# Kernel tuning notes

Measured on AMD Instinct MI355X. Metric: run time of the kernel, lower is better.

Reference implementation:

```python
import jax, jax.numpy as jnp
import numpy as np

INPUT_DIM = 64
INNER_DIM = 64
BATCH = 32768


def setup_inputs() -> dict:
    key = jax.random.key(0)
    ks = jax.random.split(key, 9)
    D, I = INPUT_DIM, INNER_DIM
    s1 = 1.0  # Linear(1, inner): fan_in=1
    s2 = 1.0 / np.sqrt(I)
    sg1 = 1.0 / np.sqrt(D * I)
    sg2 = 1.0 / np.sqrt(I)
    return {
        "x": jax.random.normal(ks[0], (BATCH, D), dtype=jnp.float32),
        # per-feature psi params, stacked over feature dim D
        "W1": jax.random.uniform(ks[1], (D, I), jnp.float32, -s1, s1),   # Linear(1, inner) weight
        "b1": jax.random.uniform(ks[2], (D, I), jnp.float32, -s1, s1),
        "W2": jax.random.uniform(ks[3], (D, I, I), jnp.float32, -s2, s2),  # Linear(inner, inner)
        "b2": jax.random.uniform(ks[4], (D, I), jnp.float32, -s2, s2),
        # g params
        "Wg1": jax.random.uniform(ks[5], (D * I, I), jnp.float32, -sg1, sg1),
        "bg1": jax.random.uniform(ks[6], (I,), jnp.float32, -sg1, sg1),
        "Wg2": jax.random.uniform(ks[7], (I, 1), jnp.float32, -sg2, sg2),
        "bg2": jax.random.uniform(ks[8], (1,), jnp.float32, -sg2, sg2),
    }


def reference(x, W1, b1, W2, b2, Wg1, bg1, Wg2, bg2):
    B = x.shape[0]
    # all psi_i first layers as one broadcasted outer product: [B, D, I]
    h = jnp.tanh(x[:, :, None] * W1[None, :, :] + b1[None, :, :])
    # per-feature second Linear(inner, inner): batched matmul over D
    psi = jnp.einsum("bdi,dio->bdo", h, W2) + b2[None, :, :]
    psi_concat = psi.reshape(B, -1)  # [B, D*I] == torch.cat over features
    hg = jnp.tanh(psi_concat @ Wg1 + bg1)
    out = hg @ Wg2 + bg2  # [B, 1]
    return out
```

## Files before the change

### kernel.cpp

```cpp
#include <hip/hip_runtime.h>
#include <stdint.h>

#define BATCH 32768
#define TANH_C 2.8853900817779268f

typedef __attribute__((ext_vector_type(8))) short short8;
typedef __attribute__((ext_vector_type(4))) float f32x4;
typedef __attribute__((ext_vector_type(4))) unsigned int u32x4;

__device__ __forceinline__ uint16_t bf16_rtne(float f) {
    union { float f; uint32_t u; } v; v.f = f;
    uint32_t u = v.u;
    u += 0x7fffu + ((u >> 16) & 1u);
    return (uint16_t)(u >> 16);
}

#if defined(__has_builtin)
#if __has_builtin(__builtin_amdgcn_cvt_pk_bf16_f32)
#define HAVE_CVT_PK_BF16 1
#endif
#endif

__device__ __forceinline__ uint32_t pack2_bf16(float a, float b) {
#ifdef HAVE_CVT_PK_BF16
    auto v = __builtin_amdgcn_cvt_pk_bf16_f32(a, b);
    uint32_t r; __builtin_memcpy(&r, &v, 4); return r;
#else
    return (uint32_t)bf16_rtne(a) | ((uint32_t)bf16_rtne(b) << 16);
#endif
}

__device__ __forceinline__ float tanh_pre(float a) {
    float e = __builtin_amdgcn_exp2f(a);
    return 1.0f - 2.0f * __builtin_amdgcn_rcpf(1.0f + e);
}

__device__ __forceinline__ float fast_tanh(float x) {
    return tanh_pre(x * TANH_C);
}

__global__ __launch_bounds__(512) void kol_pack(const float* __restrict__ W2,
                                                const float* __restrict__ Wg1,
                                                uint16_t* __restrict__ Bp) {
    __shared__ __align__(16) float w2t[64 * 65];
    __shared__ __align__(16) float g1s[64 * 64];

    const int t = threadIdx.x;
    const int d = blockIdx.x;

    for (int f = t * 4; f < 4096; f += 2048) {
        float4 v = *(const float4*)&W2[(size_t)d * 4096 + f];
        int j = f >> 6, o = f & 63;
        w2t[(o + 0) * 65 + j] = v.x;
        w2t[(o + 1) * 65 + j] = v.y;
        w2t[(o + 2) * 65 + j] = v.z;
        w2t[(o + 3) * 65 + j] = v.w;
        *(float4*)&g1s[f] = *(const float4*)&Wg1[(size_t)d * 4096 + f];
    }
    __syncthreads();

    const int jg = t >> 6;
    const int n  = t & 63;
    float acc[8];
#pragma unroll
    for (int i = 0; i < 8; ++i) acc[i] = 0.f;

#pragma unroll 4
    for (int o = 0; o < 64; ++o) {
        float g = g1s[o * 64 + n];
        const float* w = &w2t[o * 65 + jg * 8];
#pragma unroll
        for (int jj = 0; jj < 8; ++jj) acc[jj] = fmaf(w[jj], g, acc[jj]);
    }

    u32x4 pk;
    pk.x = pack2_bf16(acc[0], acc[1]);
    pk.y = pack2_bf16(acc[2], acc[3]);
    pk.z = pack2_bf16(acc[4], acc[5]);
    pk.w = pack2_bf16(acc[6], acc[7]);
    int off = ((d * 2 + (jg >> 2)) * 4 + (n >> 4)) * 64 + (jg & 3) * 16 + (n & 15);
    ((u32x4*)Bp)[off] = pk;
}

__global__ __launch_bounds__(1024) void kol_cg(const float* __restrict__ b2,
                                               const float* __restrict__ Wg1,
                                               const float* __restrict__ bg1,
                                               float* __restrict__ cg) {
    __shared__ float red[16][64];
    const int t = threadIdx.x;
    const int n = t & 63, seg = t >> 6;
    float a = 0.f;
    const int m0 = seg * 256;
#pragma unroll 4
    for (int m = m0; m < m0 + 256; ++m)
        a = fmaf(b2[m], Wg1[(size_t)m * 64 + n], a);
    red[seg][n] = a;
    __syncthreads();
    if (t < 64) {
        float s = bg1[n];
#pragma unroll
        for (int r = 0; r < 16; ++r) s += red[r][n];
        cg[n] = s;
    }
}

__global__ __launch_bounds__(512, 2) void kol_main(
    const float* __restrict__ x, const float* __restrict__ W1, const float* __restrict__ b1,
    const uint16_t* __restrict__ Bp, const float* __restrict__ cg,
    const float* __restrict__ Wg2, const float* __restrict__ bg2f,
    float* __restrict__ out) {
    __shared__ __align__(16) float xs[128 * 68];
    __shared__ __align__(16) float w1s[4096];
    __shared__ __align__(16) float b1s[4096];

    const int tid = threadIdx.x;
    const int wave = tid >> 6, lane = tid & 63;
    const int quad = lane >> 4, lm = lane & 15;
    const int rowbase = blockIdx.x * 128;

    for (int f = tid * 4; f < 8192; f += 2048) {
        int r = f >> 6, c = f & 63;
        float4 v = *(const float4*)&x[(size_t)(rowbase + r) * 64 + c];
        v.x *= TANH_C; v.y *= TANH_C; v.z *= TANH_C; v.w *= TANH_C;
        *(float4*)&xs[r * 68 + c] = v;
    }
    for (int f = tid * 4; f < 4096; f += 2048) {
        *(float4*)&w1s[f] = *(const float4*)&W1[f];
        float4 b = *(const float4*)&b1[f];
        b.x *= TANH_C; b.y *= TANH_C; b.z *= TANH_C; b.w *= TANH_C;
        *(float4*)&b1s[f] = b;
    }
    __syncthreads();

    f32x4 acc[4];
#pragma unroll
    for (int nt = 0; nt < 4; ++nt) acc[nt] = (f32x4){0.f, 0.f, 0.f, 0.f};

    const int myrow = wave * 16 + lm;
    const float* xrow = &xs[myrow * 68];
    const short8* bbase = (const short8*)Bp + lane;

    for (int d = 0; d < 64; ++d) {
        const short8* bp = bbase + (size_t)d * 8 * 64;
        short8 bf[8];
#pragma unroll
        for (int i = 0; i < 8; ++i) bf[i] = bp[i * 64];

        const float xv = xrow[d];
        const float* wq = &w1s[d * 64 + quad * 8];
        const float* bq = &b1s[d * 64 + quad * 8];
        float4 wA = *(const float4*)&wq[0];
        float4 wB = *(const float4*)&wq[4];
        float4 wC = *(const float4*)&wq[32];
        float4 wD = *(const float4*)&wq[36];
        float4 bA = *(const float4*)&bq[0];
        float4 bB = *(const float4*)&bq[4];
        float4 bC = *(const float4*)&bq[32];
        float4 bD = *(const float4*)&bq[36];

        union { short8 s; uint32_t u[4]; } a0, a1;
        a0.u[0] = pack2_bf16(tanh_pre(fmaf(xv, wA.x, bA.x)), tanh_pre(fmaf(xv, wA.y, bA.y)));
        a0.u[1] = pack2_bf16(tanh_pre(fmaf(xv, wA.z, bA.z)), tanh_pre(fmaf(xv, wA.w, bA.w)));
        a0.u[2] = pack2_bf16(tanh_pre(fmaf(xv, wB.x, bB.x)), tanh_pre(fmaf(xv, wB.y, bB.y)));
        a0.u[3] = pack2_bf16(tanh_pre(fmaf(xv, wB.z, bB.z)), tanh_pre(fmaf(xv, wB.w, bB.w)));
        a1.u[0] = pack2_bf16(tanh_pre(fmaf(xv, wC.x, bC.x)), tanh_pre(fmaf(xv, wC.y, bC.y)));
        a1.u[1] = pack2_bf16(tanh_pre(fmaf(xv, wC.z, bC.z)), tanh_pre(fmaf(xv, wC.w, bC.w)));
        a1.u[2] = pack2_bf16(tanh_pre(fmaf(xv, wD.x, bD.x)), tanh_pre(fmaf(xv, wD.y, bD.y)));
        a1.u[3] = pack2_bf16(tanh_pre(fmaf(xv, wD.z, bD.z)), tanh_pre(fmaf(xv, wD.w, bD.w)));

#pragma unroll
        for (int nt = 0; nt < 4; ++nt)
            acc[nt] = __builtin_amdgcn_mfma_f32_16x16x32_bf16(a0.s, bf[nt], acc[nt], 0, 0, 0);
#pragma unroll
        for (int nt = 0; nt < 4; ++nt)
            acc[nt] = __builtin_amdgcn_mfma_f32_16x16x32_bf16(a1.s, bf[4 + nt], acc[nt], 0, 0, 0);
    }

    float wg2v[4], cgv[4];
#pragma unroll
    for (int nt = 0; nt < 4; ++nt) {
        wg2v[nt] = Wg2[nt * 16 + lm];
        cgv[nt]  = cg[nt * 16 + lm];
    }
    const float bg2 = bg2f[0];
#pragma unroll
    for (int r = 0; r < 4; ++r) {
        float s = 0.f;
#pragma unroll
        for (int nt = 0; nt < 4; ++nt)
            s += wg2v[nt] * fast_tanh(acc[nt][r] + cgv[nt]);
        s += __shfl_xor(s, 1, 64);
        s += __shfl_xor(s, 2, 64);
        s += __shfl_xor(s, 4, 64);
        s += __shfl_xor(s, 8, 64);
        if (lm == 0) {
            int row = rowbase + wave * 16 + quad * 4 + r;
            out[row] = s + bg2;
        }
    }
}

extern "C" void kernel_launch(void* const* d_in, const int* in_sizes, int n_in,
                              void* d_out, int out_size, void* d_ws, size_t ws_size,
                              hipStream_t stream) {
    const float* x   = (const float*)d_in[0];
    const float* W1  = (const float*)d_in[1];
    const float* b1  = (const float*)d_in[2];
    const float* W2  = (const float*)d_in[3];
    const float* b2  = (const float*)d_in[4];
    const float* Wg1 = (const float*)d_in[5];
    const float* bg1 = (const float*)d_in[6];
    const float* Wg2 = (const float*)d_in[7];
    const float* bg2 = (const float*)d_in[8];
    float* out = (float*)d_out;

    uint16_t* Bp = (uint16_t*)d_ws;
    float* cg    = (float*)((char*)d_ws + 4096 * 64 * 2);

    kol_pack<<<64, 512, 0, stream>>>(W2, Wg1, Bp);
    kol_cg<<<1, 1024, 0, stream>>>(b2, Wg1, bg1, cg);
    kol_main<<<BATCH / 128, 512, 0, stream>>>(x, W1, b1, Bp, cg, Wg2, bg2, out);
}
```

Before: 150.6 us.

## Fold bias-through-Wg1 partials into pack kernel and prefetch next B fragments

```diff
diff --git a/kernel.cpp b/kernel.cpp
--- a/kernel.cpp
+++ b/kernel.cpp
@@ -41,7 +41,9 @@
 
 __global__ __launch_bounds__(512) void kol_pack(const float* __restrict__ W2,
                                                 const float* __restrict__ Wg1,
-                                                uint16_t* __restrict__ Bp) {
+                                                const float* __restrict__ b2,
+                                                uint16_t* __restrict__ Bp,
+                                                float* __restrict__ cgpart) {
     __shared__ __align__(16) float w2t[64 * 65];
     __shared__ __align__(16) float g1s[64 * 64];
 
@@ -80,28 +82,31 @@
     pk.w = pack2_bf16(acc[6], acc[7]);
     int off = ((d * 2 + (jg >> 2)) * 4 + (n >> 4)) * 64 + (jg & 3) * 16 + (n & 15);
     ((u32x4*)Bp)[off] = pk;
-}
-
-__global__ __launch_bounds__(1024) void kol_cg(const float* __restrict__ b2,
-                                               const float* __restrict__ Wg1,
-                                               const float* __restrict__ bg1,
-                                               float* __restrict__ cg) {
-    __shared__ float red[16][64];
+
+    if (t < 64) {
+        float a = 0.f;
+        const float* b2d = &b2[(size_t)d * 64];
+#pragma unroll 4
+        for (int o = 0; o < 64; ++o)
+            a = fmaf(b2d[o], g1s[o * 64 + t], a);
+        cgpart[d * 64 + t] = a;
+    }
+}
+
+__global__ __launch_bounds__(256) void kol_reduce_cg(const float* __restrict__ cgpart,
+                                                     const float* __restrict__ bg1,
+                                                     float* __restrict__ cg) {
+    __shared__ float red[4][64];
     const int t = threadIdx.x;
     const int n = t & 63, seg = t >> 6;
     float a = 0.f;
-    const int m0 = seg * 256;
 #pragma unroll 4
-    for (int m = m0; m < m0 + 256; ++m)
-        a = fmaf(b2[m], Wg1[(size_t)m * 64 + n], a);
+    for (int d = seg * 16; d < seg * 16 + 16; ++d)
+        a += cgpart[d * 64 + n];
     red[seg][n] = a;
     __syncthreads();
-    if (t < 64) {
-        float s = bg1[n];
-#pragma unroll
-        for (int r = 0; r < 16; ++r) s += red[r][n];
-        cg[n] = s;
-    }
+    if (t < 64)
+        cg[n] = bg1[n] + red[0][n] + red[1][n] + red[2][n] + red[3][n];
 }
 
 __global__ __launch_bounds__(512, 2) void kol_main(
@@ -140,11 +145,16 @@
     const float* xrow = &xs[myrow * 68];
     const short8* bbase = (const short8*)Bp + lane;
 
+    short8 bf[8];
+#pragma unroll
+    for (int i = 0; i < 8; ++i) bf[i] = bbase[i * 64];
+
+#pragma unroll 2
     for (int d = 0; d < 64; ++d) {
-        const short8* bp = bbase + (size_t)d * 8 * 64;
-        short8 bf[8];
-#pragma unroll
-        for (int i = 0; i < 8; ++i) bf[i] = bp[i * 64];
+        short8 bn[8];
+        const short8* bpn = bbase + (size_t)((d + 1) & 63) * 512;
+#pragma unroll
+        for (int i = 0; i < 8; ++i) bn[i] = bpn[i * 64];
 
         const float xv = xrow[d];
         const float* wq = &w1s[d * 64 + quad * 8];
@@ -174,6 +184,9 @@
 #pragma unroll
         for (int nt = 0; nt < 4; ++nt)
             acc[nt] = __builtin_amdgcn_mfma_f32_16x16x32_bf16(a1.s, bf[4 + nt], acc[nt], 0, 0, 0);
+
+#pragma unroll
+        for (int i = 0; i < 8; ++i) bf[i] = bn[i];
     }
 
     float wg2v[4], cgv[4];
@@ -214,10 +227,11 @@
     const float* bg2 = (const float*)d_in[8];
     float* out = (float*)d_out;
 
-    uint16_t* Bp = (uint16_t*)d_ws;
-    float* cg    = (float*)((char*)d_ws + 4096 * 64 * 2);
-
-    kol_pack<<<64, 512, 0, stream>>>(W2, Wg1, Bp);
-    kol_cg<<<1, 1024, 0, stream>>>(b2, Wg1, bg1, cg);
+    uint16_t* Bp   = (uint16_t*)d_ws;
+    float* cg      = (float*)((char*)d_ws + 4096 * 64 * 2);
+    float* cgpart  = out;
+
+    kol_pack<<<64, 512, 0, stream>>>(W2, Wg1, b2, Bp, cgpart);
+    kol_reduce_cg<<<1, 256, 0, stream>>>(cgpart, bg1, cg);
     kol_main<<<BATCH / 128, 512, 0, stream>>>(x, W1, b1, Bp, cg, Wg2, bg2, out);
 }
```

New measurement: 129.8 us. 13.8% less time.

## Split d-loop across two wave groups, fuse bias reduction, prefetch B fragments

Applied to the files above, without the earlier changes.

```diff
diff --git a/kernel.cpp b/kernel.cpp
--- a/kernel.cpp
+++ b/kernel.cpp
@@ -82,69 +82,76 @@
     ((u32x4*)Bp)[off] = pk;
 }
 
-__global__ __launch_bounds__(1024) void kol_cg(const float* __restrict__ b2,
-                                               const float* __restrict__ Wg1,
-                                               const float* __restrict__ bg1,
-                                               float* __restrict__ cg) {
-    __shared__ float red[16][64];
-    const int t = threadIdx.x;
-    const int n = t & 63, seg = t >> 6;
-    float a = 0.f;
-    const int m0 = seg * 256;
-#pragma unroll 4
-    for (int m = m0; m < m0 + 256; ++m)
-        a = fmaf(b2[m], Wg1[(size_t)m * 64 + n], a);
-    red[seg][n] = a;
-    __syncthreads();
-    if (t < 64) {
-        float s = bg1[n];
-#pragma unroll
-        for (int r = 0; r < 16; ++r) s += red[r][n];
-        cg[n] = s;
-    }
-}
-
-__global__ __launch_bounds__(512, 2) void kol_main(
+__global__ __launch_bounds__(1024, 4) void kol_main(
     const float* __restrict__ x, const float* __restrict__ W1, const float* __restrict__ b1,
-    const uint16_t* __restrict__ Bp, const float* __restrict__ cg,
+    const uint16_t* __restrict__ Bp, const float* __restrict__ b2,
+    const float* __restrict__ Wg1, const float* __restrict__ bg1,
     const float* __restrict__ Wg2, const float* __restrict__ bg2f,
     float* __restrict__ out) {
-    __shared__ __align__(16) float xs[128 * 68];
-    __shared__ __align__(16) float w1s[4096];
-    __shared__ __align__(16) float b1s[4096];
+    __shared__ __align__(16) float smem[16896];
+    float* xs  = smem;
+    float* w1s = smem + 8704;
+    float* b1s = smem + 12800;
 
     const int tid = threadIdx.x;
     const int wave = tid >> 6, lane = tid & 63;
     const int quad = lane >> 4, lm = lane & 15;
     const int rowbase = blockIdx.x * 128;
 
-    for (int f = tid * 4; f < 8192; f += 2048) {
+#pragma unroll
+    for (int ff = 0; ff < 2; ++ff) {
+        int f = tid * 4 + ff * 4096;
         int r = f >> 6, c = f & 63;
         float4 v = *(const float4*)&x[(size_t)(rowbase + r) * 64 + c];
         v.x *= TANH_C; v.y *= TANH_C; v.z *= TANH_C; v.w *= TANH_C;
         *(float4*)&xs[r * 68 + c] = v;
     }
-    for (int f = tid * 4; f < 4096; f += 2048) {
+    {
+        int f = tid * 4;
         *(float4*)&w1s[f] = *(const float4*)&W1[f];
         float4 b = *(const float4*)&b1[f];
         b.x *= TANH_C; b.y *= TANH_C; b.z *= TANH_C; b.w *= TANH_C;
         *(float4*)&b1s[f] = b;
     }
+    float cgp;
+    {
+        const int m0 = wave * 256;
+        float c0 = 0.f, c1 = 0.f, c2 = 0.f, c3 = 0.f;
+#pragma unroll 2
+        for (int m = 0; m < 256; m += 4) {
+            c0 = fmaf(b2[m0 + m + 0], Wg1[(size_t)(m0 + m + 0) * 64 + lane], c0);
+            c1 = fmaf(b2[m0 + m + 1], Wg1[(size_t)(m0 + m + 1) * 64 + lane], c1);
+            c2 = fmaf(b2[m0 + m + 2], Wg1[(size_t)(m0 + m + 2) * 64 + lane], c2);
+            c3 = fmaf(b2[m0 + m + 3], Wg1[(size_t)(m0 + m + 3) * 64 + lane], c3);
+        }
+        cgp = (c0 + c1) + (c2 + c3);
+    }
     __syncthreads();
 
     f32x4 acc[4];
 #pragma unroll
     for (int nt = 0; nt < 4; ++nt) acc[nt] = (f32x4){0.f, 0.f, 0.f, 0.f};
 
-    const int myrow = wave * 16 + lm;
+    const int w8 = wave & 7;
+    const int dlo = (wave >> 3) * 32;
+    const int myrow = w8 * 16 + lm;
     const float* xrow = &xs[myrow * 68];
     const short8* bbase = (const short8*)Bp + lane;
 
-    for (int d = 0; d < 64; ++d) {
-        const short8* bp = bbase + (size_t)d * 8 * 64;
-        short8 bf[8];
-#pragma unroll
-        for (int i = 0; i < 8; ++i) bf[i] = bp[i * 64];
+    short8 bf[8];
+    {
+        const short8* bp0 = bbase + (size_t)dlo * 512;
+#pragma unroll
+        for (int i = 0; i < 8; ++i) bf[i] = bp0[i * 64];
+    }
+
+#pragma unroll 2
+    for (int dd = 0; dd < 32; ++dd) {
+        const int d = dlo + dd;
+        short8 bn[8];
+        const short8* bpn = bbase + (size_t)((d + 1) & 63) * 512;
+#pragma unroll
+        for (int i = 0; i < 8; ++i) bn[i] = bpn[i * 64];
 
         const float xv = xrow[d];
         const float* wq = &w1s[d * 64 + quad * 8];
@@ -174,28 +181,54 @@
 #pragma unroll
         for (int nt = 0; nt < 4; ++nt)
             acc[nt] = __builtin_amdgcn_mfma_f32_16x16x32_bf16(a1.s, bf[4 + nt], acc[nt], 0, 0, 0);
-    }
-
-    float wg2v[4], cgv[4];
-#pragma unroll
-    for (int nt = 0; nt < 4; ++nt) {
-        wg2v[nt] = Wg2[nt * 16 + lm];
-        cgv[nt]  = cg[nt * 16 + lm];
-    }
-    const float bg2 = bg2f[0];
-#pragma unroll
-    for (int r = 0; r < 4; ++r) {
-        float s = 0.f;
-#pragma unroll
-        for (int nt = 0; nt < 4; ++nt)
-            s += wg2v[nt] * fast_tanh(acc[nt][r] + cgv[nt]);
-        s += __shfl_xor(s, 1, 64);
-        s += __shfl_xor(s, 2, 64);
-        s += __shfl_xor(s, 4, 64);
-        s += __shfl_xor(s, 8, 64);
-        if (lm == 0) {
-            int row = rowbase + wave * 16 + quad * 4 + r;
-            out[row] = s + bg2;
+
+#pragma unroll
+        for (int i = 0; i < 8; ++i) bf[i] = bn[i];
+    }
+
+    __syncthreads();
+    float* cmb  = xs;
+    float* part = w1s;
+    if (wave >= 8) {
+        int cb = ((wave - 8) * 64 + lane) * 16;
+#pragma unroll
+        for (int nt = 0; nt < 4; ++nt) *(f32x4*)&cmb[cb + nt * 4] = acc[nt];
+    }
+    part[wave * 64 + lane] = cgp;
+    __syncthreads();
+
+    if (wave < 8) {
+        int cb = (wave * 64 + lane) * 16;
+#pragma unroll
+        for (int nt = 0; nt < 4; ++nt) {
+            f32x4 o = *(const f32x4*)&cmb[cb + nt * 4];
+            acc[nt] = acc[nt] + o;
+        }
+        float wg2v[4], cgv[4];
+#pragma unroll
+        for (int nt = 0; nt < 4; ++nt) {
+            int n = nt * 16 + lm;
+            float c = bg1[n];
+#pragma unroll
+            for (int w = 0; w < 16; ++w) c += part[w * 64 + n];
+            cgv[nt] = c;
+            wg2v[nt] = Wg2[n];
+        }
+        const float bg2 = bg2f[0];
+#pragma unroll
+        for (int r = 0; r < 4; ++r) {
+            float s = 0.f;
+#pragma unroll
+            for (int nt = 0; nt < 4; ++nt)
+                s += wg2v[nt] * fast_tanh(acc[nt][r] + cgv[nt]);
+            s += __shfl_xor(s, 1, 64);
+            s += __shfl_xor(s, 2, 64);
+            s += __shfl_xor(s, 4, 64);
+            s += __shfl_xor(s, 8, 64);
+            if (lm == 0) {
+                int row = rowbase + w8 * 16 + quad * 4 + r;
+                out[row] = s + bg2;
+            }
         }
     }
 }
@@ -215,9 +248,7 @@
     float* out = (float*)d_out;
 
     uint16_t* Bp = (uint16_t*)d_ws;
-    float* cg    = (float*)((char*)d_ws + 4096 * 64 * 2);
 
     kol_pack<<<64, 512, 0, stream>>>(W2, Wg1, Bp);
-    kol_cg<<<1, 1024, 0, stream>>>(b2, Wg1, bg1, cg);
-    kol_main<<<BATCH / 128, 512, 0, stream>>>(x, W1, b1, Bp, cg, Wg2, bg2, out);
-}
+    kol_main<<<BATCH / 128, 1024, 0, stream>>>(x, W1, b1, Bp, b2, Wg1, bg1, Wg2, bg2, out);
+}
```

Result: faster. 140.0 us (-7.0%).
